# Performance work log

Hardware: AMD Instinct MI355X
Metric: run time of the kernel (lower is better)

The kernel has to match this reference:

```python
import jax, jax.numpy as jnp
import numpy as np

# dims: NL layers, D=d_model, DI=expand*D, F=d_ff, V=vocab, L=S*C seq, R=dt_rank, N=d_state, K=d_conv
NL, D, DI, F, V, L, R, N, K = 2, 256, 512, 1024, 1024, 1024, 16, 16, 4
B, S, C = 2, 128, 8
EPS = 1e-5


def silu(x):
    return x * jax.nn.sigmoid(x)


def batchnorm(x, g, b):  # x: [B,L,D], normalize over (B,L) per channel (training-mode BatchNorm1d)
    m = x.mean((0, 1))
    v = x.var((0, 1))
    return (x - m) * jax.lax.rsqrt(v + EPS) * g + b


def layernorm(x, g, b):
    m = x.mean(-1, keepdims=True)
    v = x.var(-1, keepdims=True)
    return (x - m) * jax.lax.rsqrt(v + EPS) * g + b


def mamba(x, Win, cw, cb, Wx, Wdt, bdt, A_log, Dsk, Wout, bout):
    # x: [B,L,D] -> [B,L,D]; standard Mamba block with selective scan
    Bsz, Lseq, _ = x.shape
    xz = x @ Win                      # [B,L,2*DI]
    xi, z = jnp.split(xz, 2, axis=-1)
    # depthwise causal conv1d, width K
    xp = jnp.pad(xi, ((0, 0), (K - 1, 0), (0, 0)))
    xc = cb + sum(xp[:, k:k + Lseq, :] * cw[:, k] for k in range(K))
    xc = silu(xc)                     # [B,L,DI]
    xdb = xc @ Wx                     # [B,L,R+2N]
    delta = jax.nn.softplus(xdb[..., :R] @ Wdt + bdt)   # [B,L,DI]
    Bm = xdb[..., R:R + N]            # [B,L,N]
    Cm = xdb[..., R + N:]             # [B,L,N]
    A = -jnp.exp(A_log)               # [DI,N]
    dA = jnp.exp(delta[..., None] * A)                       # [B,L,DI,N]
    dBx = delta[..., None] * Bm[:, :, None, :] * xc[..., None]  # [B,L,DI,N]

    def step(h, inp):
        dA_t, dBx_t, C_t = inp
        h = h * dA_t + dBx_t          # [B,DI,N]
        y = jnp.einsum('bdn,bn->bd', h, C_t)
        return h, y

    h0 = jnp.zeros((Bsz, DI, N), x.dtype)
    _, ys = jax.lax.scan(step, h0, (dA.transpose(1, 0, 2, 3), dBx.transpose(1, 0, 2, 3), Cm.transpose(1, 0, 2)))
    y = ys.transpose(1, 0, 2) + Dsk * xc
    y = y * silu(z)
    return y @ Wout + bout


def _forward(input_ids, emb, pos, Win, conv_w, conv_b, Wx, Wdt, bdt, A_log, Dskip, Wout, bout,
             bn_g, bn_b, ln_g, ln_b, ff_w1, ff_b1, ff_w2, ff_b2, final_w, final_b):
    Bsz, Ssz, Csz = input_ids.shape
    Lseq = Ssz * Csz
    # Encoder: token embedding (scaled) + learned positions, flattened to [B, S*C, D]
    x = emb[input_ids].reshape(Bsz, Lseq, D) * jnp.sqrt(jnp.float32(D)) + pos[:Lseq]
    for i in range(NL):
        f = mamba(x, Win[i, 0], conv_w[i, 0], conv_b[i, 0], Wx[i, 0], Wdt[i, 0], bdt[i, 0],
                  A_log[i, 0], Dskip[i, 0], Wout[i, 0], bout[i, 0])
        f = batchnorm(f, bn_g[i, 0], bn_b[i, 0])
        bk = mamba(x[:, ::-1], Win[i, 1], conv_w[i, 1], conv_b[i, 1], Wx[i, 1], Wdt[i, 1], bdt[i, 1],
                   A_log[i, 1], Dskip[i, 1], Wout[i, 1], bout[i, 1])
        bk = batchnorm(bk, bn_g[i, 1], bn_b[i, 1])[:, ::-1]
        f = layernorm(x + f, ln_g[i, 0], ln_b[i, 0])
        bk = layernorm(x + bk, ln_g[i, 1], ln_b[i, 1])
        out = f + bk
        out = jax.nn.relu(out @ ff_w1[i] + ff_b1[i]) @ ff_w2[i] + ff_b2[i]
        out = batchnorm(out, bn_g[i, 2], bn_b[i, 2])
        x = out + x
    return x.reshape(Bsz, Ssz, Csz, D) @ final_w + final_b   # [B,S,C,V]


def setup_inputs() -> dict:
    key = jax.random.key(0)
    ks = list(jax.random.split(key, 16))
    kit = iter(ks)
    rn = lambda shape, s=0.02: jax.random.normal(next(kit), shape, jnp.float32) * s
    inp = {
        'input_ids': jax.random.randint(next(kit), (B, S, C), 0, V),
        'emb': rn((V, D)), 'pos': rn((L, D)),
        'Win': rn((NL, 2, D, 2 * DI)),
        'conv_w': rn((NL, 2, DI, K), 0.1), 'conv_b': jnp.zeros((NL, 2, DI)),
        'Wx': rn((NL, 2, DI, R + 2 * N)),
        'Wdt': rn((NL, 2, R, DI)), 'bdt': jnp.full((NL, 2, DI), -4.0),
        'A_log': jnp.broadcast_to(jnp.log(jnp.arange(1, N + 1, dtype=jnp.float32)), (NL, 2, DI, N)) + 0.0,
        'Dskip': jnp.ones((NL, 2, DI)),
        'Wout': rn((NL, 2, DI, D)), 'bout': jnp.zeros((NL, 2, D)),
        'bn_g': jnp.ones((NL, 3, D)), 'bn_b': jnp.zeros((NL, 3, D)),
        'ln_g': jnp.ones((NL, 2, D)), 'ln_b': jnp.zeros((NL, 2, D)),
        'ff_w1': rn((NL, D, F)), 'ff_b1': jnp.zeros((NL, F)),
        'ff_w2': rn((NL, F, D)), 'ff_b2': jnp.zeros((NL, D)),
        'final_w': rn((D, V)), 'final_b': jnp.zeros((V,)),
    }
    return inp


def reference(input_ids, emb, pos, Win, conv_w, conv_b, Wx, Wdt, bdt, A_log, Dskip, Wout, bout,
              bn_g, bn_b, ln_g, ln_b, ff_w1, ff_b1, ff_w2, ff_b2, final_w, final_b):
    return _forward(input_ids, emb, pos, Win, conv_w, conv_b, Wx, Wdt, bdt, A_log, Dskip, Wout, bout,
                    bn_g, bn_b, ln_g, ln_b, ff_w1, ff_b1, ff_w2, ff_b2, final_w, final_b)
```

## Files before the change

kernel.cpp:

```cpp
#include <hip/hip_runtime.h>

#define NL 2
#define DMODEL 256
#define DI 512
#define FF 1024
#define VV 1024
#define LSEQ 1024
#define RR 16
#define NN 16
#define KCONV 4
#define BTOK 2048
#define EPS 1e-5f

using short8 = __attribute__((ext_vector_type(8))) short;
using float4v = __attribute__((ext_vector_type(4))) float;
typedef unsigned short u16;

__device__ inline float bf2f(u16 u) {
    union { unsigned u; float f; } x; x.u = (unsigned)u << 16; return x.f;
}
__device__ inline u16 f2bf(float f) {
    union { float f; unsigned u; } x; x.f = f;
    unsigned r = x.u + 0x7fffu + ((x.u >> 16) & 1u);
    return (u16)(r >> 16);
}

#if __has_builtin(__builtin_amdgcn_exp2f)
#define EXP2(x) __builtin_amdgcn_exp2f(x)
#else
#define EXP2(x) exp2f(x)
#endif

struct TMat { const float* src; u16* dst; int rows, cols, tile0, tilecols; };
struct TTable { TMat m[24]; int nmat; };

__global__ __launch_bounds__(256) void transpose_kernel(TTable tt) {
    __shared__ u16 tile[32][33];
    int bx = blockIdx.x;
    int j = 0;
    for (int k = 1; k < tt.nmat; ++k) if (bx >= tt.m[k].tile0) j = k;
    TMat mm = tt.m[j];
    int lt = bx - mm.tile0;
    int r0 = (lt / mm.tilecols) * 32, c0 = (lt % mm.tilecols) * 32;
    int tx = threadIdx.x & 31, ty = threadIdx.x >> 5;
    #pragma unroll
    for (int k = 0; k < 4; ++k) {
        int r = r0 + ty + k * 8, c = c0 + tx;
        tile[ty + k * 8][tx] = (r < mm.rows && c < mm.cols) ? f2bf(mm.src[(size_t)r * mm.cols + c]) : (u16)0;
    }
    __syncthreads();
    #pragma unroll
    for (int k = 0; k < 4; ++k) {
        int c = c0 + ty + k * 8, r = r0 + tx;
        if (c < mm.cols && r < mm.rows) mm.dst[(size_t)c * mm.rows + r] = tile[tx][ty + k * 8];
    }
}

__global__ __launch_bounds__(256) void gemm_kernel(
    const u16* __restrict__ A0, int lda, unsigned long long sA,
    const u16* __restrict__ B0, int ldb, unsigned long long sB,
    const float* __restrict__ bias0, unsigned long long sBias,
    void* __restrict__ C0, int ldc, unsigned long long sC,
    int M, int N, int K, int act, int outfp)
{
    const u16* A = A0 + (size_t)blockIdx.z * sA;
    const u16* Bt = B0 + (size_t)blockIdx.z * sB;
    const float* bias = bias0 ? (bias0 + (size_t)blockIdx.z * sBias) : nullptr;

    int tid = threadIdx.x;
    int wv = tid >> 6, lane = tid & 63;
    int row0 = blockIdx.y * 64 + (wv >> 1) * 32;
    int col0 = blockIdx.x * 64 + (wv & 1) * 32;
    int mi = lane & 15, kq = lane >> 4;

    float4v acc[2][2];
    #pragma unroll
    for (int a = 0; a < 2; ++a)
        #pragma unroll
        for (int b = 0; b < 2; ++b) acc[a][b] = (float4v){0.f, 0.f, 0.f, 0.f};
    const short8 zer = {0, 0, 0, 0, 0, 0, 0, 0};

    for (int kk = 0; kk < K; kk += 32) {
        int k = kk + kq * 8;
        bool kv = (k < K);
        short8 af[2], bf[2];
        #pragma unroll
        for (int rt = 0; rt < 2; ++rt) {
            int r = row0 + rt * 16 + mi;
            af[rt] = kv ? *(const short8*)(A + (size_t)r * lda + k) : zer;
        }
        #pragma unroll
        for (int ct = 0; ct < 2; ++ct) {
            int n = col0 + ct * 16 + mi;
            bf[ct] = (kv && n < N) ? *(const short8*)(Bt + (size_t)n * ldb + k) : zer;
        }
        #pragma unroll
        for (int rt = 0; rt < 2; ++rt)
            #pragma unroll
            for (int ct = 0; ct < 2; ++ct)
                acc[rt][ct] = __builtin_amdgcn_mfma_f32_16x16x32_bf16(af[rt], bf[ct], acc[rt][ct], 0, 0, 0);
    }

    #pragma unroll
    for (int rt = 0; rt < 2; ++rt)
        #pragma unroll
        for (int ct = 0; ct < 2; ++ct) {
            int n = col0 + ct * 16 + mi;
            if (n >= N) continue;
            float bv = bias ? bias[n] : 0.f;
            #pragma unroll
            for (int r = 0; r < 4; ++r) {
                int m = row0 + rt * 16 + kq * 4 + r;
                float v = acc[rt][ct][r] + bv;
                if (act == 1) v = fmaxf(v, 0.f);
                if (outfp)
                    ((float*)C0)[(size_t)blockIdx.z * sC + (size_t)m * ldc + n] = v;
                else
                    ((u16*)C0)[(size_t)blockIdx.z * sC + (size_t)m * ldc + n] = f2bf(v);
            }
        }
}

__global__ __launch_bounds__(256) void delta_fused_kernel(
    const u16* __restrict__ xdb, const u16* __restrict__ wdtT,
    const float* __restrict__ bdt, const u16* __restrict__ xc,
    u16* __restrict__ deltaT, u16* __restrict__ uT, int layer)
{
    int z = blockIdx.z;
    const u16* A = xdb + (size_t)z * BTOK * 48;
    const u16* Bt = wdtT + (size_t)z * 512 * 16;
    const float* bias = bdt + (size_t)z * 512;

    int tid = threadIdx.x;
    int wv = tid >> 6, lane = tid & 63;
    int row0 = blockIdx.y * 64 + (wv >> 1) * 32;
    int col0 = blockIdx.x * 64 + (wv & 1) * 32;
    int mi = lane & 15, kq = lane >> 4;

    float4v acc[2][2];
    #pragma unroll
    for (int a = 0; a < 2; ++a)
        #pragma unroll
        for (int b = 0; b < 2; ++b) acc[a][b] = (float4v){0.f, 0.f, 0.f, 0.f};
    const short8 zer = {0, 0, 0, 0, 0, 0, 0, 0};

    int k = kq * 8;
    bool kv = (k < 16);
    short8 af[2], bf[2];
    #pragma unroll
    for (int rt = 0; rt < 2; ++rt) {
        int r = row0 + rt * 16 + mi;
        af[rt] = kv ? *(const short8*)(A + (size_t)r * 48 + k) : zer;
    }
    #pragma unroll
    for (int ct = 0; ct < 2; ++ct) {
        int n = col0 + ct * 16 + mi;
        bf[ct] = kv ? *(const short8*)(Bt + (size_t)n * 16 + k) : zer;
    }
    #pragma unroll
    for (int rt = 0; rt < 2; ++rt)
        #pragma unroll
        for (int ct = 0; ct < 2; ++ct)
            acc[rt][ct] = __builtin_amdgcn_mfma_f32_16x16x32_bf16(af[rt], bf[ct], acc[rt][ct], 0, 0, 0);

    #pragma unroll
    for (int rt = 0; rt < 2; ++rt)
        #pragma unroll
        for (int ct = 0; ct < 2; ++ct) {
            int n = col0 + ct * 16 + mi;
            float bv = bias[n];
            #pragma unroll
            for (int r = 0; r < 4; ++r) {
                int m = row0 + rt * 16 + kq * 4 + r;
                float v = acc[rt][ct][r] + bv;
                v = (v > 20.f) ? v : logf(1.f + __expf(v));
                float xcv = bf2f(xc[((size_t)z * BTOK + m) * DI + n]);
                int b = m >> 10, t = m & 1023;
                size_t off = ((size_t)((z * 2 + b) * DI + n)) * LSEQ + t;
                deltaT[off] = f2bf(v);
                uT[off] = f2bf(v * xcv);
            }
        }
}

__global__ __launch_bounds__(256) void embed_kernel(
    const int* __restrict__ ids, const float* __restrict__ emb,
    const float* __restrict__ pos, u16* __restrict__ x)
{
    int tok = blockIdx.x, d = threadIdx.x;
    int id = ids[tok];
    float v = emb[(size_t)id * DMODEL + d] * 16.0f + pos[(size_t)(tok & (LSEQ - 1)) * DMODEL + d];
    x[(size_t)tok * DMODEL + d] = f2bf(v);
}

__global__ __launch_bounds__(256) void conv_kernel(
    const u16* __restrict__ xz, const float* __restrict__ conv_w,
    const float* __restrict__ conv_b, u16* __restrict__ xc, int layer)
{
    unsigned g = blockIdx.x * 256u + threadIdx.x;
    int d = g & 511;
    int t = (g >> 9) & 1023;
    int b = (g >> 19) & 1;
    int dir = g >> 20;
    int wbase = ((layer * 2 + dir) * DI + d);
    float acc = conv_b[wbase];
    int colbase = dir * 1024 + d;
    #pragma unroll
    for (int k = 0; k < KCONV; ++k) {
        int ts = dir ? (t + 3 - k) : (t - 3 + k);
        if (ts >= 0 && ts < LSEQ)
            acc += conv_w[wbase * KCONV + k] * bf2f(xz[(size_t)((b << 10) + ts) * 2048 + colbase]);
    }
    float v = acc / (1.f + __expf(-acc));
    xc[(size_t)(((dir * 2 + b) << 10) + t) * DI + d] = f2bf(v);
}

template<int DIR>
__device__ __forceinline__ void scan_body(
    const u16* __restrict__ deltaT, const u16* __restrict__ uT,
    const u16* __restrict__ xdb, const float* __restrict__ A_log,
    u16* __restrict__ pT, int layer, int slab,
    float* Ps, float* Qs)
{
    int c = threadIdx.x;
    int d = blockIdx.x;

    float a2[16];
    const float* al = A_log + (size_t)(((layer * 2 + DIR) * DI + d) * NN);
    #pragma unroll
    for (int n = 0; n < 16; ++n) a2[n] = -__expf(al[n]) * 1.44269504f;

    const size_t tb = ((size_t)(slab * DI + d)) * LSEQ;
    const int rowb = slab << 10;
    const int T0 = DIR ? (1016 - 8 * c) : (8 * c);

    short8 dlv = *(const short8*)(deltaT + tb + T0);
    short8 uvv = *(const short8*)(uT + tb + T0);

    float P[16], Q[16];
    #pragma unroll
    for (int n = 0; n < 16; ++n) { P[n] = 1.f; Q[n] = 0.f; }
    #pragma unroll
    for (int j = 0; j < 8; ++j) {
        const int idx = DIR ? 7 - j : j;
        float dl = bf2f((u16)dlv[idx]);
        float uv = bf2f((u16)uvv[idx]);
        const u16* xr = xdb + (size_t)(rowb + T0 + idx) * 48;
        short8 b0 = *(const short8*)(xr + 16);
        short8 b1 = *(const short8*)(xr + 24);
        #pragma unroll
        for (int n = 0; n < 8; ++n) {
            float dA = EXP2(dl * a2[n]);
            Q[n] = Q[n] * dA + uv * bf2f((u16)b0[n]);
            P[n] *= dA;
        }
        #pragma unroll
        for (int n = 0; n < 8; ++n) {
            float dA = EXP2(dl * a2[8 + n]);
            Q[8 + n] = Q[8 + n] * dA + uv * bf2f((u16)b1[n]);
            P[8 + n] *= dA;
        }
    }
    const int base = c * 17;
    #pragma unroll
    for (int n = 0; n < 16; ++n) { Ps[base + n] = P[n]; Qs[base + n] = Q[n]; }
    __syncthreads();

    for (int off = 1; off < 128; off <<= 1) {
        float pp[16], qp[16];
        const bool act = (c >= off);
        if (act) {
            int nb = (c - off) * 17;
            #pragma unroll
            for (int n = 0; n < 16; ++n) { pp[n] = Ps[nb + n]; qp[n] = Qs[nb + n]; }
        }
        __syncthreads();
        if (act) {
            #pragma unroll
            for (int n = 0; n < 16; ++n) {
                Q[n] = fmaf(P[n], qp[n], Q[n]);
                P[n] *= pp[n];
                Ps[base + n] = P[n];
                Qs[base + n] = Q[n];
            }
        }
        __syncthreads();
    }

    float h[16];
    if (c == 0) {
        #pragma unroll
        for (int n = 0; n < 16; ++n) h[n] = 0.f;
    } else {
        int nb = (c - 1) * 17;
        #pragma unroll
        for (int n = 0; n < 16; ++n) h[n] = Qs[nb + n];
    }

    short8 pk;
    #pragma unroll
    for (int j = 0; j < 8; ++j) {
        const int idx = DIR ? 7 - j : j;
        float dl = bf2f((u16)dlv[idx]);
        float uv = bf2f((u16)uvv[idx]);
        const u16* xr = xdb + (size_t)(rowb + T0 + idx) * 48;
        short8 b0 = *(const short8*)(xr + 16);
        short8 b1 = *(const short8*)(xr + 24);
        short8 c0 = *(const short8*)(xr + 32);
        short8 c1 = *(const short8*)(xr + 40);
        float pacc[4] = {0.f, 0.f, 0.f, 0.f};
        #pragma unroll
        for (int n = 0; n < 8; ++n) {
            float dA = EXP2(dl * a2[n]);
            h[n] = h[n] * dA + uv * bf2f((u16)b0[n]);
            pacc[n & 3] = fmaf(h[n], bf2f((u16)c0[n]), pacc[n & 3]);
        }
        #pragma unroll
        for (int n = 0; n < 8; ++n) {
            float dA = EXP2(dl * a2[8 + n]);
            h[8 + n] = h[8 + n] * dA + uv * bf2f((u16)b1[n]);
            pacc[n & 3] = fmaf(h[8 + n], bf2f((u16)c1[n]), pacc[n & 3]);
        }
        pk[idx] = (short)f2bf((pacc[0] + pacc[1]) + (pacc[2] + pacc[3]));
    }
    *(short8*)(pT + tb + T0) = pk;
}

__global__ __launch_bounds__(128) void scan_kernel(
    const u16* __restrict__ deltaT, const u16* __restrict__ uT,
    const u16* __restrict__ xdb, const float* __restrict__ A_log,
    u16* __restrict__ pT, int layer)
{
    __shared__ float Ps[128 * 17], Qs[128 * 17];
    int slab = blockIdx.y;
    if (slab >> 1)
        scan_body<1>(deltaT, uT, xdb, A_log, pT, layer, slab, Ps, Qs);
    else
        scan_body<0>(deltaT, uT, xdb, A_log, pT, layer, slab, Ps, Qs);
}

__global__ __launch_bounds__(256) void gate_kernel(
    const u16* __restrict__ pT, const u16* __restrict__ xc,
    const u16* __restrict__ xz, const float* __restrict__ Dskip,
    u16* __restrict__ y, int layer)
{
    __shared__ float tile[32][33];
    int z = blockIdx.z, dir = z >> 1, b = z & 1;
    int d0 = blockIdx.x * 32, t0 = blockIdx.y * 32;
    int tx = threadIdx.x & 31, ty = threadIdx.x >> 5;
    #pragma unroll
    for (int k = 0; k < 4; ++k) {
        int d = d0 + ty + k * 8;
        tile[ty + k * 8][tx] = bf2f(pT[((size_t)(z * DI + d)) * LSEQ + t0 + tx]);
    }
    __syncthreads();
    #pragma unroll
    for (int k = 0; k < 4; ++k) {
        int t = t0 + ty + k * 8, d = d0 + tx;
        float p = tile[tx][ty + k * 8];
        float xcv = bf2f(xc[(size_t)((z << 10) + t) * DI + d]);
        float zv = bf2f(xz[(size_t)((b << 10) + t) * 2048 + dir * 1024 + 512 + d]);
        float dsk = Dskip[(layer * 2 + dir) * DI + d];
        float yv = (p + dsk * xcv) * (zv / (1.f + __expf(-zv)));
        y[(size_t)((z << 10) + t) * DI + d] = f2bf(yv);
    }
}

__global__ __launch_bounds__(256) void bnstats_kernel(
    const u16* __restrict__ p0, const u16* __restrict__ p1, float* __restrict__ stats)
{
    int d = blockIdx.x, arr = blockIdx.y, tid = threadIdx.x;
    const u16* p = arr ? p1 : p0;
    float s = 0.f, q = 0.f;
    #pragma unroll
    for (int k = 0; k < 8; ++k) {
        float v = bf2f(p[(size_t)(tid + k * 256) * DMODEL + d]);
        s += v; q += v * v;
    }
    #pragma unroll
    for (int off = 1; off < 64; off <<= 1) { s += __shfl_xor(s, off); q += __shfl_xor(q, off); }
    __shared__ float ss[4], qs[4];
    if ((tid & 63) == 0) { ss[tid >> 6] = s; qs[tid >> 6] = q; }
    __syncthreads();
    if (tid == 0) {
        float S = ss[0] + ss[1] + ss[2] + ss[3];
        float Q2 = qs[0] + qs[1] + qs[2] + qs[3];
        float mean = S * (1.f / 2048.f);
        float var = Q2 * (1.f / 2048.f) - mean * mean;
        stats[(arr * DMODEL + d) * 2] = mean;
        stats[(arr * DMODEL + d) * 2 + 1] = rsqrtf(var + EPS);
    }
}

__global__ __launch_bounds__(256) void fuseln_kernel(
    const u16* __restrict__ x, const u16* __restrict__ outm, const float* __restrict__ stats,
    const float* __restrict__ bng, const float* __restrict__ bnb,
    const float* __restrict__ lng, const float* __restrict__ lnb, u16* __restrict__ ffin)
{
    int tok = blockIdx.x, d = threadIdx.x;
    float xv = bf2f(x[(size_t)tok * DMODEL + d]);
    float of = bf2f(outm[(size_t)tok * DMODEL + d]);
    float ob = bf2f(outm[(size_t)BTOK * DMODEL + (size_t)tok * DMODEL + d]);
    float vf = xv + (of - stats[d * 2]) * stats[d * 2 + 1] * bng[d] + bnb[d];
    float vb = xv + (ob - stats[(DMODEL + d) * 2]) * stats[(DMODEL + d) * 2 + 1] * bng[DMODEL + d] + bnb[DMODEL + d];
    float s0 = vf, s1 = vf * vf, s2 = vb, s3 = vb * vb;
    #pragma unroll
    for (int off = 1; off < 64; off <<= 1) {
        s0 += __shfl_xor(s0, off); s1 += __shfl_xor(s1, off);
        s2 += __shfl_xor(s2, off); s3 += __shfl_xor(s3, off);
    }
    __shared__ float sm[4][4];
    if ((d & 63) == 0) { sm[d >> 6][0] = s0; sm[d >> 6][1] = s1; sm[d >> 6][2] = s2; sm[d >> 6][3] = s3; }
    __syncthreads();
    s0 = sm[0][0] + sm[1][0] + sm[2][0] + sm[3][0];
    s1 = sm[0][1] + sm[1][1] + sm[2][1] + sm[3][1];
    s2 = sm[0][2] + sm[1][2] + sm[2][2] + sm[3][2];
    s3 = sm[0][3] + sm[1][3] + sm[2][3] + sm[3][3];
    float mf = s0 * (1.f / 256.f), vvf = s1 * (1.f / 256.f) - mf * mf;
    float mb = s2 * (1.f / 256.f), vvb = s3 * (1.f / 256.f) - mb * mb;
    float fl = (vf - mf) * rsqrtf(vvf + EPS) * lng[d] + lnb[d];
    float bl = (vb - mb) * rsqrtf(vvb + EPS) * lng[DMODEL + d] + lnb[DMODEL + d];
    ffin[(size_t)tok * DMODEL + d] = f2bf(fl + bl);
}

__global__ __launch_bounds__(256) void bnadd_kernel(
    u16* __restrict__ x, const u16* __restrict__ ffo, const float* __restrict__ stats,
    const float* __restrict__ g, const float* __restrict__ b)
{
    int tok = blockIdx.x, d = threadIdx.x;
    size_t idx = (size_t)tok * DMODEL + d;
    float v = bf2f(x[idx]) + (bf2f(ffo[idx]) - stats[d * 2]) * stats[d * 2 + 1] * g[d] + b[d];
    x[idx] = f2bf(v);
}

extern "C" void kernel_launch(void* const* d_in, const int* in_sizes, int n_in,
                              void* d_out, int out_size, void* d_ws, size_t ws_size,
                              hipStream_t stream)
{
    const int*   ids     = (const int*)d_in[0];
    const float* emb     = (const float*)d_in[1];
    const float* pos     = (const float*)d_in[2];
    const float* Win     = (const float*)d_in[3];
    const float* conv_w  = (const float*)d_in[4];
    const float* conv_b  = (const float*)d_in[5];
    const float* Wx      = (const float*)d_in[6];
    const float* Wdt     = (const float*)d_in[7];
    const float* bdt     = (const float*)d_in[8];
    const float* A_log   = (const float*)d_in[9];
    const float* Dskip   = (const float*)d_in[10];
    const float* Wout    = (const float*)d_in[11];
    const float* bout    = (const float*)d_in[12];
    const float* bn_g    = (const float*)d_in[13];
    const float* bn_b    = (const float*)d_in[14];
    const float* ln_g    = (const float*)d_in[15];
    const float* ln_b    = (const float*)d_in[16];
    const float* ff_w1   = (const float*)d_in[17];
    const float* ff_b1   = (const float*)d_in[18];
    const float* ff_w2   = (const float*)d_in[19];
    const float* ff_b2   = (const float*)d_in[20];
    const float* final_w = (const float*)d_in[21];
    const float* final_b = (const float*)d_in[22];

    char* cur = (char*)d_ws;
    auto alloc = [&](size_t elems) {
        u16* p = (u16*)cur;
        cur += ((elems * 2 + 511) / 512) * 512;
        return p;
    };
    u16* winT  = alloc((size_t)NL * 2048 * 256);
    u16* wxT   = alloc((size_t)NL * 2 * 48 * 512);
    u16* wdtT  = alloc((size_t)NL * 2 * 512 * 16);
    u16* woutT = alloc((size_t)NL * 2 * 256 * 512);
    u16* fw1T  = alloc((size_t)NL * 1024 * 256);
    u16* fw2T  = alloc((size_t)NL * 256 * 1024);
    u16* finT  = alloc((size_t)1024 * 256);
    u16* xbuf   = alloc((size_t)BTOK * DMODEL);
    u16* xz     = alloc((size_t)BTOK * 2048);
    u16* xc     = alloc((size_t)2 * BTOK * DI);
    u16* xdb    = alloc((size_t)2 * BTOK * 48);
    u16* deltaT = alloc((size_t)2 * BTOK * DI);
    u16* uT     = alloc((size_t)2 * BTOK * DI);
    u16* pT     = alloc((size_t)2 * BTOK * DI);
    u16* ybuf   = alloc((size_t)2 * BTOK * DI);
    u16* outm   = alloc((size_t)2 * BTOK * DMODEL);
    u16* ffin   = alloc((size_t)BTOK * DMODEL);
    u16* ffh    = alloc((size_t)BTOK * FF);
    u16* ffo    = alloc((size_t)BTOK * DMODEL);
    float* statsM = (float*)alloc(4096);
    float* statsF = statsM + 1024;

    TTable tt; int nm = 0, tiles = 0;
    auto addT = [&](const float* src, u16* dst, int rows, int cols) {
        int tc = (cols + 31) / 32, tr = (rows + 31) / 32;
        tt.m[nm] = {src, dst, rows, cols, tiles, tc};
        tiles += tc * tr; nm++;
    };
    for (int i = 0; i < NL; ++i) {
        for (int dir = 0; dir < 2; ++dir) {
            addT(Win  + (size_t)(i * 2 + dir) * 256 * 1024, winT  + (size_t)i * 2048 * 256 + (size_t)dir * 1024 * 256, 256, 1024);
            addT(Wx   + (size_t)(i * 2 + dir) * 512 * 48,   wxT   + (size_t)(i * 2 + dir) * 48 * 512,   512, 48);
            addT(Wdt  + (size_t)(i * 2 + dir) * 16 * 512,   wdtT  + (size_t)(i * 2 + dir) * 512 * 16,   16, 512);
            addT(Wout + (size_t)(i * 2 + dir) * 512 * 256,  woutT + (size_t)(i * 2 + dir) * 256 * 512,  512, 256);
        }
        addT(ff_w1 + (size_t)i * 256 * 1024, fw1T + (size_t)i * 1024 * 256, 256, 1024);
        addT(ff_w2 + (size_t)i * 1024 * 256, fw2T + (size_t)i * 256 * 1024, 1024, 256);
    }
    addT(final_w, finT, 256, 1024);
    tt.nmat = nm;
    transpose_kernel<<<tiles, 256, 0, stream>>>(tt);

    embed_kernel<<<BTOK, 256, 0, stream>>>(ids, emb, pos, xbuf);

    auto gemm = [&](const u16* A, int lda, size_t sA, const u16* Bt, int ldb, size_t sB,
                    const float* bias, size_t sBias, void* C, int ldc, size_t sC,
                    int M, int N, int K, int act, int nb, int outfp) {
        dim3 g((N + 63) / 64, M / 64, nb);
        gemm_kernel<<<g, 256, 0, stream>>>(A, lda, (unsigned long long)sA, Bt, ldb, (unsigned long long)sB,
                                           bias, (unsigned long long)sBias, C, ldc, (unsigned long long)sC,
                                           M, N, K, act, outfp);
    };

    for (int i = 0; i < NL; ++i) {
        gemm(xbuf, 256, 0, winT + (size_t)i * 2048 * 256, 256, 0, nullptr, 0,
             xz, 2048, 0, BTOK, 2048, 256, 0, 1, 0);
        conv_kernel<<<(2 * BTOK * DI) / 256, 256, 0, stream>>>(xz, conv_w, conv_b, xc, i);
        gemm(xc, 512, (size_t)BTOK * 512, wxT + (size_t)i * 2 * 48 * 512, 512, 48 * 512,
             nullptr, 0, xdb, 48, (size_t)BTOK * 48, BTOK, 48, 512, 0, 2, 0);
        delta_fused_kernel<<<dim3(8, 32, 2), 256, 0, stream>>>(
            xdb, wdtT + (size_t)i * 2 * 512 * 16, bdt + (size_t)i * 2 * 512, xc, deltaT, uT, i);
        scan_kernel<<<dim3(512, 4), 128, 0, stream>>>(deltaT, uT, xdb, A_log, pT, i);
        gate_kernel<<<dim3(DI / 32, LSEQ / 32, 4), 256, 0, stream>>>(pT, xc, xz, Dskip, ybuf, i);
        gemm(ybuf, 512, (size_t)BTOK * 512, woutT + (size_t)i * 2 * 256 * 512, 512, 256 * 512,
             bout + (size_t)i * 2 * 256, 256, outm, 256, (size_t)BTOK * 256, BTOK, 256, 512, 0, 2, 0);
        bnstats_kernel<<<dim3(256, 2), 256, 0, stream>>>(outm, outm + (size_t)BTOK * 256, statsM);
        fuseln_kernel<<<BTOK, 256, 0, stream>>>(xbuf, outm, statsM,
            bn_g + (size_t)i * 3 * 256, bn_b + (size_t)i * 3 * 256,
            ln_g + (size_t)i * 2 * 256, ln_b + (size_t)i * 2 * 256, ffin);
        gemm(ffin, 256, 0, fw1T + (size_t)i * 1024 * 256, 256, 0,
             ff_b1 + (size_t)i * 1024, 0, ffh, 1024, 0, BTOK, 1024, 256, 1, 1, 0);
        gemm(ffh, 1024, 0, fw2T + (size_t)i * 256 * 1024, 1024, 0,
             ff_b2 + (size_t)i * 256, 0, ffo, 256, 0, BTOK, 256, 1024, 0, 1, 0);
        bnstats_kernel<<<dim3(256, 1), 256, 0, stream>>>(ffo, ffo, statsF);
        bnadd_kernel<<<BTOK, 256, 0, stream>>>(xbuf, ffo, statsF,
            bn_g + (size_t)(i * 3 + 2) * 256, bn_b + (size_t)(i * 3 + 2) * 256);
    }
    gemm(xbuf, 256, 0, finT, 256, 0, final_b, 0,
         d_out, 1024, 0, BTOK, 1024, 256, 0, 1, 1);
}
```

Baseline: 444.9 us.

## Transpose B/C scan inputs to time-major layout and loop scan per state

Result: faster. 433.6 us (-2.5%).

```diff
diff --git a/kernel.cpp b/kernel.cpp
--- a/kernel.cpp
+++ b/kernel.cpp
@@ -183,6 +183,26 @@
         }
 }
 
+__global__ __launch_bounds__(256) void bct_kernel(
+    const u16* __restrict__ xdb, u16* __restrict__ bcT)
+{
+    __shared__ u16 tile[32][34];
+    int slab = blockIdx.y;
+    int t0 = blockIdx.x * 32;
+    int tx = threadIdx.x & 31, ty = threadIdx.x >> 5;
+    #pragma unroll
+    for (int k = 0; k < 4; ++k) {
+        int t = t0 + ty + k * 8;
+        tile[tx][ty + k * 8] = xdb[(size_t)(slab * 1024 + t) * 48 + 16 + tx];
+    }
+    __syncthreads();
+    #pragma unroll
+    for (int k = 0; k < 4; ++k) {
+        int col = ty + k * 8;
+        bcT[((size_t)(slab * 32 + col)) * LSEQ + t0 + tx] = tile[col][tx];
+    }
+}
+
 __global__ __launch_bounds__(256) void embed_kernel(
     const int* __restrict__ ids, const float* __restrict__ emb,
     const float* __restrict__ pos, u16* __restrict__ x)
@@ -218,12 +238,12 @@
 template<int DIR>
 __device__ __forceinline__ void scan_body(
     const u16* __restrict__ deltaT, const u16* __restrict__ uT,
-    const u16* __restrict__ xdb, const float* __restrict__ A_log,
+    const u16* __restrict__ bcT, const float* __restrict__ A_log,
     u16* __restrict__ pT, int layer, int slab,
     float* Ps, float* Qs)
 {
-    int c = threadIdx.x;
-    int d = blockIdx.x;
+    const int c = threadIdx.x;
+    const int d = blockIdx.x;
 
     float a2[16];
     const float* al = A_log + (size_t)(((layer * 2 + DIR) * DI + d) * NN);
@@ -231,112 +251,93 @@
     for (int n = 0; n < 16; ++n) a2[n] = -__expf(al[n]) * 1.44269504f;
 
     const size_t tb = ((size_t)(slab * DI + d)) * LSEQ;
-    const int rowb = slab << 10;
+    const size_t bcb = (size_t)slab * 32 * LSEQ;
     const int T0 = DIR ? (1016 - 8 * c) : (8 * c);
 
     short8 dlv = *(const short8*)(deltaT + tb + T0);
     short8 uvv = *(const short8*)(uT + tb + T0);
-
-    float P[16], Q[16];
-    #pragma unroll
-    for (int n = 0; n < 16; ++n) { P[n] = 1.f; Q[n] = 0.f; }
-    #pragma unroll
-    for (int j = 0; j < 8; ++j) {
-        const int idx = DIR ? 7 - j : j;
-        float dl = bf2f((u16)dlv[idx]);
-        float uv = bf2f((u16)uvv[idx]);
-        const u16* xr = xdb + (size_t)(rowb + T0 + idx) * 48;
-        short8 b0 = *(const short8*)(xr + 16);
-        short8 b1 = *(const short8*)(xr + 24);
-        #pragma unroll
-        for (int n = 0; n < 8; ++n) {
-            float dA = EXP2(dl * a2[n]);
-            Q[n] = Q[n] * dA + uv * bf2f((u16)b0[n]);
-            P[n] *= dA;
-        }
-        #pragma unroll
-        for (int n = 0; n < 8; ++n) {
-            float dA = EXP2(dl * a2[8 + n]);
-            Q[8 + n] = Q[8 + n] * dA + uv * bf2f((u16)b1[n]);
-            P[8 + n] *= dA;
-        }
-    }
+    float dls[8], uvs[8];
+    #pragma unroll
+    for (int s = 0; s < 8; ++s) {
+        const int idx = DIR ? 7 - s : s;
+        dls[s] = bf2f((u16)dlv[idx]);
+        uvs[s] = bf2f((u16)uvv[idx]);
+    }
+
     const int base = c * 17;
     #pragma unroll
-    for (int n = 0; n < 16; ++n) { Ps[base + n] = P[n]; Qs[base + n] = Q[n]; }
+    for (int n = 0; n < 16; ++n) {
+        short8 B8 = *(const short8*)(bcT + bcb + (size_t)n * LSEQ + T0);
+        float P = 1.f, Q = 0.f;
+        #pragma unroll
+        for (int s = 0; s < 8; ++s) {
+            const int idx = DIR ? 7 - s : s;
+            float dA = EXP2(dls[s] * a2[n]);
+            Q = Q * dA + uvs[s] * bf2f((u16)B8[idx]);
+            P *= dA;
+        }
+        Ps[base + n] = P;
+        Qs[base + n] = Q;
+    }
     __syncthreads();
 
     for (int off = 1; off < 128; off <<= 1) {
-        float pp[16], qp[16];
+        float np[16], nq[16];
         const bool act = (c >= off);
         if (act) {
-            int nb = (c - off) * 17;
+            const int nb = (c - off) * 17;
             #pragma unroll
-            for (int n = 0; n < 16; ++n) { pp[n] = Ps[nb + n]; qp[n] = Qs[nb + n]; }
+            for (int n = 0; n < 16; ++n) { np[n] = Ps[nb + n]; nq[n] = Qs[nb + n]; }
         }
         __syncthreads();
         if (act) {
             #pragma unroll
             for (int n = 0; n < 16; ++n) {
-                Q[n] = fmaf(P[n], qp[n], Q[n]);
-                P[n] *= pp[n];
-                Ps[base + n] = P[n];
-                Qs[base + n] = Q[n];
+                float p = Ps[base + n], q = Qs[base + n];
+                Qs[base + n] = fmaf(p, nq[n], q);
+                Ps[base + n] = p * np[n];
             }
         }
         __syncthreads();
     }
 
-    float h[16];
-    if (c == 0) {
-        #pragma unroll
-        for (int n = 0; n < 16; ++n) h[n] = 0.f;
-    } else {
-        int nb = (c - 1) * 17;
-        #pragma unroll
-        for (int n = 0; n < 16; ++n) h[n] = Qs[nb + n];
-    }
-
+    float pacc[8];
+    #pragma unroll
+    for (int s = 0; s < 8; ++s) pacc[s] = 0.f;
+    const int hb = (c - 1) * 17;
+    #pragma unroll
+    for (int n = 0; n < 16; ++n) {
+        short8 B8 = *(const short8*)(bcT + bcb + (size_t)n * LSEQ + T0);
+        short8 C8 = *(const short8*)(bcT + bcb + (size_t)(16 + n) * LSEQ + T0);
+        float h = (c == 0) ? 0.f : Qs[hb + n];
+        #pragma unroll
+        for (int s = 0; s < 8; ++s) {
+            const int idx = DIR ? 7 - s : s;
+            float dA = EXP2(dls[s] * a2[n]);
+            h = h * dA + uvs[s] * bf2f((u16)B8[idx]);
+            pacc[s] = fmaf(h, bf2f((u16)C8[idx]), pacc[s]);
+        }
+    }
     short8 pk;
     #pragma unroll
-    for (int j = 0; j < 8; ++j) {
-        const int idx = DIR ? 7 - j : j;
-        float dl = bf2f((u16)dlv[idx]);
-        float uv = bf2f((u16)uvv[idx]);
-        const u16* xr = xdb + (size_t)(rowb + T0 + idx) * 48;
-        short8 b0 = *(const short8*)(xr + 16);
-        short8 b1 = *(const short8*)(xr + 24);
-        short8 c0 = *(const short8*)(xr + 32);
-        short8 c1 = *(const short8*)(xr + 40);
-        float pacc[4] = {0.f, 0.f, 0.f, 0.f};
-        #pragma unroll
-        for (int n = 0; n < 8; ++n) {
-            float dA = EXP2(dl * a2[n]);
-            h[n] = h[n] * dA + uv * bf2f((u16)b0[n]);
-            pacc[n & 3] = fmaf(h[n], bf2f((u16)c0[n]), pacc[n & 3]);
-        }
-        #pragma unroll
-        for (int n = 0; n < 8; ++n) {
-            float dA = EXP2(dl * a2[8 + n]);
-            h[8 + n] = h[8 + n] * dA + uv * bf2f((u16)b1[n]);
-            pacc[n & 3] = fmaf(h[8 + n], bf2f((u16)c1[n]), pacc[n & 3]);
-        }
-        pk[idx] = (short)f2bf((pacc[0] + pacc[1]) + (pacc[2] + pacc[3]));
+    for (int s = 0; s < 8; ++s) {
+        const int idx = DIR ? 7 - s : s;
+        pk[idx] = (short)f2bf(pacc[s]);
     }
     *(short8*)(pT + tb + T0) = pk;
 }
 
 __global__ __launch_bounds__(128) void scan_kernel(
     const u16* __restrict__ deltaT, const u16* __restrict__ uT,
-    const u16* __restrict__ xdb, const float* __restrict__ A_log,
+    const u16* __restrict__ bcT, const float* __restrict__ A_log,
     u16* __restrict__ pT, int layer)
 {
     __shared__ float Ps[128 * 17], Qs[128 * 17];
     int slab = blockIdx.y;
     if (slab >> 1)
-        scan_body<1>(deltaT, uT, xdb, A_log, pT, layer, slab, Ps, Qs);
+        scan_body<1>(deltaT, uT, bcT, A_log, pT, layer, slab, Ps, Qs);
     else
-        scan_body<0>(deltaT, uT, xdb, A_log, pT, layer, slab, Ps, Qs);
+        scan_body<0>(deltaT, uT, bcT, A_log, pT, layer, slab, Ps, Qs);
 }
 
 __global__ __launch_bounds__(256) void gate_kernel(
@@ -478,6 +479,7 @@
     u16* xz     = alloc((size_t)BTOK * 2048);
     u16* xc     = alloc((size_t)2 * BTOK * DI);
     u16* xdb    = alloc((size_t)2 * BTOK * 48);
+    u16* bcT    = alloc((size_t)4 * 32 * LSEQ);
     u16* deltaT = alloc((size_t)2 * BTOK * DI);
     u16* uT     = alloc((size_t)2 * BTOK * DI);
     u16* pT     = alloc((size_t)2 * BTOK * DI);
@@ -526,9 +528,10 @@
         conv_kernel<<<(2 * BTOK * DI) / 256, 256, 0, stream>>>(xz, conv_w, conv_b, xc, i);
         gemm(xc, 512, (size_t)BTOK * 512, wxT + (size_t)i * 2 * 48 * 512, 512, 48 * 512,
              nullptr, 0, xdb, 48, (size_t)BTOK * 48, BTOK, 48, 512, 0, 2, 0);
+        bct_kernel<<<dim3(32, 4), 256, 0, stream>>>(xdb, bcT);
         delta_fused_kernel<<<dim3(8, 32, 2), 256, 0, stream>>>(
             xdb, wdtT + (size_t)i * 2 * 512 * 16, bdt + (size_t)i * 2 * 512, xc, deltaT, uT, i);
-        scan_kernel<<<dim3(512, 4), 128, 0, stream>>>(deltaT, uT, xdb, A_log, pT, i);
+        scan_kernel<<<dim3(512, 4), 128, 0, stream>>>(deltaT, uT, bcT, A_log, pT, i);
         gate_kernel<<<dim3(DI / 32, LSEQ / 32, 4), 256, 0, stream>>>(pT, xc, xz, Dskip, ybuf, i);
         gemm(ybuf, 512, (size_t)BTOK * 512, woutT + (size_t)i * 2 * 256 * 512, 512, 256 * 512,
              bout + (size_t)i * 2 * 256, 256, outm, 256, (size_t)BTOK * 256, BTOK, 256, 512, 0, 2, 0);
```
